# Kernel tuning notes

Measured on AMD Instinct MI355X. Metric: run time of the kernel, lower is better.

## Reference

```python
import jax, jax.numpy as jnp
import numpy as np

N_NODES = 100000
N_EDGES = 800000
F_IN, HID, N_CLS = 256, 128, 32


def setup_inputs() -> dict:
    key = jax.random.key(0)
    k1, k2, k3, k4, k5 = jax.random.split(key, 5)
    features = jax.random.normal(k1, (N_NODES, F_IN), dtype=jnp.float32)
    # random directed edges with no self loops (so add_remaining_self_loops == append all loops)
    src = jax.random.randint(k2, (N_EDGES,), 0, N_NODES)
    off = jax.random.randint(k3, (N_EDGES,), 1, N_NODES)
    dst = (src + off) % N_NODES
    edge_index = jnp.stack([src, dst]).astype(jnp.int64)
    # Glorot-style params for the two GCNConv layers
    W1 = jax.random.normal(k4, (F_IN, HID), dtype=jnp.float32) * (1.0 / np.sqrt(F_IN))
    b1 = jnp.zeros((HID,), dtype=jnp.float32)
    W2 = jax.random.normal(k5, (HID, N_CLS), dtype=jnp.float32) * (1.0 / np.sqrt(HID))
    b2 = jnp.zeros((N_CLS,), dtype=jnp.float32)
    return {"features": features, "edge_index": edge_index, "W1": W1, "b1": b1, "W2": W2, "b2": b2}


def _gcn_conv(x, W, b, src, dst, norm, n):
    xw = x @ W                                  # [N, d_out] dense GEMM
    msg = xw[src] * norm[:, None]               # gather + scale, [E, d_out]
    out = jax.ops.segment_sum(msg, dst, num_segments=n)  # scatter-add to targets
    return out + b


def reference(features, edge_index, W1, b1, W2, b2):
    n = features.shape[0]
    # add_remaining_self_loops (input has none, so append all)
    loops = jnp.arange(n, dtype=edge_index.dtype)
    src = jnp.concatenate([edge_index[0], loops])
    dst = jnp.concatenate([edge_index[1], loops])
    # gcn_norm: deg over targets, sym normalization deg^-1/2 A deg^-1/2
    deg = jax.ops.segment_sum(jnp.ones_like(src, dtype=features.dtype), dst, num_segments=n)
    dinv = jnp.where(deg > 0, jax.lax.rsqrt(deg), 0.0)
    norm = dinv[src] * dinv[dst]
    x = _gcn_conv(features, W1, b1, src, dst, norm, n)
    x = jax.nn.relu(x)
    # dropout is identity at inference (training=False)
    x = _gcn_conv(x, W2, b2, src, dst, norm, n)
    return jax.nn.log_softmax(x, axis=1)
```

## Files before the change

### kernel.cpp

```cpp
#include <hip/hip_runtime.h>
#include <hip/hip_bf16.h>

typedef __bf16 bf16_t;
typedef __attribute__((ext_vector_type(8))) __bf16 bf16x8;
typedef __attribute__((ext_vector_type(4))) float f32x4;
typedef __attribute__((ext_vector_type(2))) float f32x2;

__device__ inline void packB_one(const float* __restrict__ B, bf16_t* __restrict__ Bp,
                                 int N, int idx) {
    int j    = idx & 7;
    int lane = (idx >> 3) & 63;
    int st   = idx >> 9;
    int nt   = N >> 4;
    int s = st / nt, t = st - s * nt;
    int k = s * 32 + (lane >> 4) * 8 + j;
    int n = t * 16 + (lane & 15);
    Bp[idx] = (bf16_t)B[(size_t)k * N + n];
}

__device__ inline void fma8_fp8(uint2 u, float w, float* a) {
    f32x2 p;
    p = __builtin_amdgcn_cvt_pk_f32_fp8(u.x, false); a[0] += p[0] * w; a[1] += p[1] * w;
    p = __builtin_amdgcn_cvt_pk_f32_fp8(u.x, true);  a[2] += p[0] * w; a[3] += p[1] * w;
    p = __builtin_amdgcn_cvt_pk_f32_fp8(u.y, false); a[4] += p[0] * w; a[5] += p[1] * w;
    p = __builtin_amdgcn_cvt_pk_f32_fp8(u.y, true);  a[6] += p[0] * w; a[7] += p[1] * w;
}

__global__ __launch_bounds__(256) void k_prep(
        const float* __restrict__ W1, bf16_t* __restrict__ Bp1,
        const float* __restrict__ W2, bf16_t* __restrict__ Bp2,
        int* __restrict__ deg, int N) {
    int b = blockIdx.x, t = threadIdx.x;
    const int PACKB = (32768 + 4096) / 256;
    if (b < PACKB) {
        int idx = b * 256 + t;
        if (idx < 32768) packB_one(W1, Bp1, 128, idx);
        else             packB_one(W2, Bp2, 32, idx - 32768);
        return;
    }
    int i = ((b - PACKB) * 256 + t) * 4;
    if (i < N) {
        if (i + 4 <= N) *(int4*)(deg + i) = make_int4(0, 0, 0, 0);
        else for (int j = 0; i + j < N; ++j) deg[i + j] = 0;
    }
}

template <int KSTEPS, int NTILES>
__global__ __launch_bounds__(256) void k_front(
        const float* __restrict__ feat, const bf16_t* __restrict__ Bp1,
        unsigned char* __restrict__ XW1, int M,
        const int* __restrict__ dst, int* __restrict__ deg,
        int* __restrict__ rank, int E, int DEGB) {
    int b = blockIdx.x, t = threadIdx.x;
    if (b < DEGB) {
        int i = b * 1024 + t * 4;
        if (i + 4 <= E) {
            int4 v = *(const int4*)(dst + i);
            int4 r;
            r.x = atomicAdd(&deg[v.x], 1);
            r.y = atomicAdd(&deg[v.y], 1);
            r.z = atomicAdd(&deg[v.z], 1);
            r.w = atomicAdd(&deg[v.w], 1);
            *(int4*)(rank + i) = r;
        } else {
            for (int j = 0; j < 4; ++j)
                if (i + j < E) rank[i + j] = atomicAdd(&deg[dst[i + j]], 1);
        }
        return;
    }
    b -= DEGB;
    {
        int wave = (b * 256 + t) >> 6;
        if (wave * 16 >= M) return;
        int lane = t & 63;
        int r16 = lane & 15, quad = lane >> 4;
        const int K = KSTEPS * 32, N = NTILES * 16;
        f32x4 acc[NTILES] = {};
        const float* arow = feat + (size_t)(wave * 16 + r16) * K + quad * 8;
#pragma unroll
        for (int s = 0; s < KSTEPS; ++s) {
            const float* ap = arow + s * 32;
            bf16x8 a;
#pragma unroll
            for (int j = 0; j < 8; ++j) a[j] = (bf16_t)ap[j];
            const bf16_t* bp = Bp1 + ((size_t)(s * NTILES) * 64 + lane) * 8;
#pragma unroll
            for (int tt = 0; tt < NTILES; ++tt) {
                bf16x8 bb = *(const bf16x8*)(bp + tt * 512);
                acc[tt] = __builtin_amdgcn_mfma_f32_16x16x32_bf16(a, bb, acc[tt], 0, 0, 0);
            }
        }
#pragma unroll
        for (int tt = 0; tt < NTILES; ++tt)
#pragma unroll
            for (int r = 0; r < 4; ++r) {
                int pk = __builtin_amdgcn_cvt_pk_fp8_f32(acc[tt][r], acc[tt][r], 0, false);
                XW1[(size_t)(wave * 16 + quad * 4 + r) * N + tt * 16 + r16] =
                    (unsigned char)pk;
            }
    }
}

__global__ __launch_bounds__(256) void k_dinv_scan1(const int* __restrict__ deg,
                                                    float* __restrict__ dinv,
                                                    int* __restrict__ bsum, int n) {
    __shared__ int red[256];
    int b = blockIdx.x, t = threadIdx.x;
    int base = b * 1024 + t * 4;
    int s = 0;
#pragma unroll
    for (int j = 0; j < 4; ++j) {
        int i = base + j;
        if (i < n) { int d = deg[i]; s += d; dinv[i] = rsqrtf((float)(d + 1)); }
    }
    red[t] = s;
    __syncthreads();
    for (int d = 128; d > 0; d >>= 1) {
        if (t < d) red[t] += red[t + d];
        __syncthreads();
    }
    if (t == 0) bsum[b] = red[0];
}

__global__ __launch_bounds__(256) void k_scan3f(const int* __restrict__ deg,
                                                const int* __restrict__ bsum, int nb,
                                                int* __restrict__ rowPtr, int n) {
    __shared__ int red[256];
    __shared__ int boff[256];
    int b = blockIdx.x, t = threadIdx.x;
    int base = b * 1024 + t * 4;
    int v[4]; int s = 0;
#pragma unroll
    for (int j = 0; j < 4; ++j) { int i = base + j; v[j] = (i < n) ? deg[i] : 0; s += v[j]; }
    red[t] = s;
    boff[t] = (t < nb) ? bsum[t] : 0;
    __syncthreads();
    for (int d = 1; d < 256; d <<= 1) {
        int u  = (t >= d) ? red[t - d]  : 0;
        int u2 = (t >= d) ? boff[t - d] : 0;
        __syncthreads();
        red[t] += u;
        boff[t] += u2;
        __syncthreads();
    }
    int blockOff = (b == 0) ? 0 : boff[b - 1];
    if (b == 0 && t == 0) rowPtr[n] = boff[nb - 1];
    int run = blockOff + red[t] - s;
#pragma unroll
    for (int j = 0; j < 4; ++j) {
        int i = base + j;
        if (i < n) { rowPtr[i] = run; run += v[j]; }
    }
}

__global__ __launch_bounds__(256) void k_scatter(
        const int* __restrict__ src, const int* __restrict__ dst,
        const int* __restrict__ rank, const int* __restrict__ rowPtr,
        const float* __restrict__ dinv, int2* __restrict__ edata, int E) {
    int i = (blockIdx.x * 256 + threadIdx.x) * 4;
    if (i + 4 <= E) {
        int4 s4 = *(const int4*)(src + i);
        int4 d4 = *(const int4*)(dst + i);
        int4 r4 = *(const int4*)(rank + i);
        int p0 = rowPtr[d4.x] + r4.x, p1 = rowPtr[d4.y] + r4.y;
        int p2 = rowPtr[d4.z] + r4.z, p3 = rowPtr[d4.w] + r4.w;
        int2 e0; e0.x = s4.x; e0.y = __float_as_int(dinv[s4.x] * dinv[d4.x]);
        int2 e1; e1.x = s4.y; e1.y = __float_as_int(dinv[s4.y] * dinv[d4.y]);
        int2 e2; e2.x = s4.z; e2.y = __float_as_int(dinv[s4.z] * dinv[d4.z]);
        int2 e3; e3.x = s4.w; e3.y = __float_as_int(dinv[s4.w] * dinv[d4.w]);
        edata[p0] = e0; edata[p1] = e1; edata[p2] = e2; edata[p3] = e3;
    } else {
        for (int j = 0; j < 4; ++j) {
            int e = i + j;
            if (e >= E) break;
            int s = src[e], d = dst[e];
            int2 p; p.x = s; p.y = __float_as_int(dinv[s] * dinv[d]);
            edata[rowPtr[d] + rank[e]] = p;
        }
    }
}

template <int KSTEPS, int NTILES>
__global__ __launch_bounds__(256) void k_gemm_p(
        const bf16_t* __restrict__ Ap, const bf16_t* __restrict__ Bp,
        bf16_t* __restrict__ C, int M) {
    int wave = (blockIdx.x * blockDim.x + threadIdx.x) >> 6;
    if (wave * 16 >= M) return;
    int lane = threadIdx.x & 63;
    int r16 = lane & 15, quad = lane >> 4;
    const int N = NTILES * 16;
    f32x4 acc[NTILES] = {};
    const bf16_t* apb = Ap + (size_t)wave * (KSTEPS * 512) + lane * 8;
#pragma unroll
    for (int s = 0; s < KSTEPS; ++s) {
        bf16x8 a = *(const bf16x8*)(apb + s * 512);
        const bf16_t* bp = Bp + ((size_t)(s * NTILES) * 64 + lane) * 8;
#pragma unroll
        for (int t = 0; t < NTILES; ++t) {
            bf16x8 b = *(const bf16x8*)(bp + t * 512);
            acc[t] = __builtin_amdgcn_mfma_f32_16x16x32_bf16(a, b, acc[t], 0, 0, 0);
        }
    }
#pragma unroll
    for (int t = 0; t < NTILES; ++t)
#pragma unroll
        for (int r = 0; r < 4; ++r)
            C[(size_t)(wave * 16 + quad * 4 + r) * N + t * 16 + r16] = (bf16_t)acc[t][r];
}

__global__ __launch_bounds__(256) void k_agg1(
        const int* __restrict__ rowPtr, const int2* __restrict__ edata,
        const unsigned char* __restrict__ XW1, const float* __restrict__ dinv,
        const float* __restrict__ b1, bf16_t* __restrict__ Hp, int n) {
    int wave = (blockIdx.x * blockDim.x + threadIdx.x) >> 6;
    if (wave >= n) return;
    int lane = threadIdx.x & 63;
    int fl = (lane & 15) << 3;
    int h  = lane >> 4;
    int r0 = rowPtr[wave], r1 = rowPtr[wave + 1];
    float d = dinv[wave], d2 = d * d;
    uint2 us = *(const uint2*)(XW1 + (size_t)wave * 128 + fl);
    float a0[8] = {}, a1[8] = {};
    int k = r0 + h;
    for (; k + 4 < r1; k += 8) {
        int2 e0 = edata[k], e1 = edata[k + 4];
        float w0 = __int_as_float(e0.y), w1 = __int_as_float(e1.y);
        uint2 u0 = *(const uint2*)(XW1 + (size_t)e0.x * 128 + fl);
        uint2 u1 = *(const uint2*)(XW1 + (size_t)e1.x * 128 + fl);
        fma8_fp8(u0, w0, a0);
        fma8_fp8(u1, w1, a1);
    }
    if (k < r1) {
        int2 e0 = edata[k];
        float w0 = __int_as_float(e0.y);
        uint2 u0 = *(const uint2*)(XW1 + (size_t)e0.x * 128 + fl);
        fma8_fp8(u0, w0, a0);
    }
#pragma unroll
    for (int j = 0; j < 8; ++j) {
        a0[j] += a1[j];
        a0[j] += __shfl_xor(a0[j], 16);
        a0[j] += __shfl_xor(a0[j], 32);
    }
    if (h == 0) {
        fma8_fp8(us, d2, a0);
        bf16x8 hv;
#pragma unroll
        for (int j = 0; j < 8; ++j) {
            float v = a0[j] + b1[fl + j];
            hv[j] = (bf16_t)fmaxf(v, 0.f);
        }
        int q = lane & 15;
        size_t off = (((size_t)(wave >> 4) * 4 + (q >> 2)) * 64
                      + (wave & 15) + 16 * (q & 3)) * 8;
        *(bf16x8*)(Hp + off) = hv;
    }
}

__global__ __launch_bounds__(256) void k_agg2(
        const int* __restrict__ rowPtr, const int2* __restrict__ edata,
        const bf16_t* __restrict__ XW2, const float* __restrict__ dinv,
        const float* __restrict__ b2, float* __restrict__ out, int n) {
    int wave = (blockIdx.x * blockDim.x + threadIdx.x) >> 6;
    if (wave >= n) return;
    int lane = threadIdx.x & 63;
    int g = lane & 15;
    int h = lane >> 4;
    int r0 = rowPtr[wave], r1 = rowPtr[wave + 1];
    float d = dinv[wave], d2 = d * d;
    unsigned ps = *(const unsigned*)(XW2 + ((size_t)wave << 5) + 2 * g);
    float2 bb = *(const float2*)(b2 + 2 * g);
    float a00 = 0.f, a01 = 0.f, a10 = 0.f, a11 = 0.f;
    int k = r0 + h;
    for (; k + 4 < r1; k += 8) {
        int2 e0 = edata[k], e1 = edata[k + 4];
        float w0 = __int_as_float(e0.y), w1 = __int_as_float(e1.y);
        unsigned p0 = *(const unsigned*)(XW2 + ((size_t)e0.x << 5) + 2 * g);
        unsigned p1 = *(const unsigned*)(XW2 + ((size_t)e1.x << 5) + 2 * g);
        a00 += __int_as_float(p0 << 16) * w0;
        a01 += __int_as_float(p0 & 0xffff0000u) * w0;
        a10 += __int_as_float(p1 << 16) * w1;
        a11 += __int_as_float(p1 & 0xffff0000u) * w1;
    }
    if (k < r1) {
        int2 e0 = edata[k];
        float w0 = __int_as_float(e0.y);
        unsigned p0 = *(const unsigned*)(XW2 + ((size_t)e0.x << 5) + 2 * g);
        a00 += __int_as_float(p0 << 16) * w0;
        a01 += __int_as_float(p0 & 0xffff0000u) * w0;
    }
    float v0 = a00 + a10, v1 = a01 + a11;
    v0 += __shfl_xor(v0, 16); v0 += __shfl_xor(v0, 32);
    v1 += __shfl_xor(v1, 16); v1 += __shfl_xor(v1, 32);
    v0 += __int_as_float(ps << 16) * d2 + bb.x;
    v1 += __int_as_float(ps & 0xffff0000u) * d2 + bb.y;
    float mx = fmaxf(v0, v1);
#pragma unroll
    for (int m = 8; m >= 1; m >>= 1) mx = fmaxf(mx, __shfl_xor(mx, m));
    float s = __expf(v0 - mx) + __expf(v1 - mx);
#pragma unroll
    for (int m = 8; m >= 1; m >>= 1) s += __shfl_xor(s, m);
    if (h == 0) {
        float ls = __logf(s);
        float2 o; o.x = v0 - mx - ls; o.y = v1 - mx - ls;
        *(float2*)(out + ((size_t)wave << 5) + 2 * g) = o;
    }
}

extern "C" void kernel_launch(void* const* d_in, const int* in_sizes, int n_in,
                              void* d_out, int out_size, void* d_ws, size_t ws_size,
                              hipStream_t stream) {
    const float* feat = (const float*)d_in[0];
    const int*   eidx = (const int*)d_in[1];
    const float* W1   = (const float*)d_in[2];
    const float* b1   = (const float*)d_in[3];
    const float* W2   = (const float*)d_in[4];
    const float* b2   = (const float*)d_in[5];
    float* out = (float*)d_out;

    const int FIN = 256, HID = 128, NCLS = 32;
    const int N = in_sizes[0] / FIN;
    const int E = in_sizes[1] / 2;
    const int* src = eidx;
    const int* dst = eidx + E;

    char* ws = (char*)d_ws;
    size_t o = 0;
    auto alloc = [&](size_t bytes) -> void* {
        void* p = ws + o;
        o = (o + bytes + 255) & ~(size_t)255;
        return p;
    };
    int*    deg    = (int*)   alloc((size_t)N * 4);
    int*    rank   = (int*)   alloc((size_t)E * 4);
    float*  dinv   = (float*) alloc((size_t)N * 4);
    int*    rowPtr = (int*)   alloc((size_t)(N + 1) * 4);
    int*    bsum   = (int*)   alloc(256 * 4);
    bf16_t* Bp1    = (bf16_t*)alloc((size_t)(FIN / 32) * (HID / 16) * 512 * 2);
    bf16_t* Bp2    = (bf16_t*)alloc((size_t)(HID / 32) * (NCLS / 16) * 512 * 2);
    int2*   edata  = (int2*)  alloc((size_t)E * 8);
    unsigned char* XW1 = (unsigned char*)alloc((size_t)N * HID);
    bf16_t* Hp     = (bf16_t*)alloc((size_t)N * HID * 2);
    bf16_t* XW2    = (bf16_t*)XW1;

    const int T = 256;
    const int NB = (N + 1023) >> 10;
    const int DEGB  = (E + 1023) / 1024;
    const int GEMMB = (((N + 15) / 16) * 64 + T - 1) / T;
    const int PACKB = (32768 + 4096) / 256;
    const int ZB    = (N + 1023) / 1024;

    k_prep      <<<PACKB + ZB, T, 0, stream>>>(W1, Bp1, W2, Bp2, deg, N);
    k_front<8, 8><<<DEGB + GEMMB, T, 0, stream>>>(
        feat, Bp1, XW1, N, dst, deg, rank, E, DEGB);
    k_dinv_scan1<<<NB, T, 0, stream>>>(deg, dinv, bsum, N);
    k_scan3f    <<<NB, T, 0, stream>>>(deg, bsum, NB, rowPtr, N);
    k_scatter   <<<(E + 1023) / 1024, T, 0, stream>>>(src, dst, rank, rowPtr, dinv, edata, E);
    k_agg1<<<(N * 64 + T - 1) / T, T, 0, stream>>>(rowPtr, edata, XW1, dinv, b1, Hp, N);
    {
        int waves = (N + 15) / 16;
        k_gemm_p<4, 2><<<(waves * 64 + T - 1) / T, T, 0, stream>>>(Hp, Bp2, XW2, N);
    }
    k_agg2<<<(N * 64 + T - 1) / T, T, 0, stream>>>(rowPtr, edata, XW2, dinv, b2, out, N);
}
```

Baseline: 317.8 us.

## Privatize degree counters per XCC to use workgroup-scope atomics

Degree counting now keeps eight private copies of the degree array, one per XCC, selected by reading the hardware XCC id. The atomics run at workgroup scope so they can resolve in the local L2 instead of going device-wide. The XCC id is tagged into the high bits of each rank, and a later pass prefix-sums the per-XCC counts into offsets used during scatter. This adds an 8x larger zeroing and reading pass plus extra gathers in scatter, and it depends on workgroup-scope atomics staying coherent within one XCC's L2.

```diff
diff --git a/kernel.cpp b/kernel.cpp
--- a/kernel.cpp
+++ b/kernel.cpp
@@ -5,6 +5,15 @@
 typedef __attribute__((ext_vector_type(8))) __bf16 bf16x8;
 typedef __attribute__((ext_vector_type(4))) float f32x4;
 typedef __attribute__((ext_vector_type(2))) float f32x2;
+
+__device__ inline int xcc_id() {
+    int x;
+    asm volatile("s_getreg_b32 %0, hwreg(20, 0, 32)" : "=s"(x));
+    return x & 7;
+}
+__device__ inline int l2AtomicAdd(int* p, int v) {
+    return __hip_atomic_fetch_add(p, v, __ATOMIC_RELAXED, __HIP_MEMORY_SCOPE_WORKGROUP);
+}
 
 __device__ inline void packB_one(const float* __restrict__ B, bf16_t* __restrict__ Bp,
                                  int N, int idx) {
@@ -29,7 +38,7 @@
 __global__ __launch_bounds__(256) void k_prep(
         const float* __restrict__ W1, bf16_t* __restrict__ Bp1,
         const float* __restrict__ W2, bf16_t* __restrict__ Bp2,
-        int* __restrict__ deg, int N) {
+        int* __restrict__ deg8, int n8) {
     int b = blockIdx.x, t = threadIdx.x;
     const int PACKB = (32768 + 4096) / 256;
     if (b < PACKB) {
@@ -39,9 +48,9 @@
         return;
     }
     int i = ((b - PACKB) * 256 + t) * 4;
-    if (i < N) {
-        if (i + 4 <= N) *(int4*)(deg + i) = make_int4(0, 0, 0, 0);
-        else for (int j = 0; i + j < N; ++j) deg[i + j] = 0;
+    if (i < n8) {
+        if (i + 4 <= n8) *(int4*)(deg8 + i) = make_int4(0, 0, 0, 0);
+        else for (int j = 0; i + j < n8; ++j) deg8[i + j] = 0;
     }
 }
 
@@ -49,22 +58,25 @@
 __global__ __launch_bounds__(256) void k_front(
         const float* __restrict__ feat, const bf16_t* __restrict__ Bp1,
         unsigned char* __restrict__ XW1, int M,
-        const int* __restrict__ dst, int* __restrict__ deg,
-        int* __restrict__ rank, int E, int DEGB) {
+        const int* __restrict__ dst, int* __restrict__ deg8,
+        int* __restrict__ rank, int Nn, int E, int DEGB) {
     int b = blockIdx.x, t = threadIdx.x;
     if (b < DEGB) {
+        int x = xcc_id();
+        int* degx = deg8 + (size_t)x * Nn;
+        int tag = x << 28;
         int i = b * 1024 + t * 4;
         if (i + 4 <= E) {
             int4 v = *(const int4*)(dst + i);
             int4 r;
-            r.x = atomicAdd(&deg[v.x], 1);
-            r.y = atomicAdd(&deg[v.y], 1);
-            r.z = atomicAdd(&deg[v.z], 1);
-            r.w = atomicAdd(&deg[v.w], 1);
+            r.x = l2AtomicAdd(&degx[v.x], 1) | tag;
+            r.y = l2AtomicAdd(&degx[v.y], 1) | tag;
+            r.z = l2AtomicAdd(&degx[v.z], 1) | tag;
+            r.w = l2AtomicAdd(&degx[v.w], 1) | tag;
             *(int4*)(rank + i) = r;
         } else {
             for (int j = 0; j < 4; ++j)
-                if (i + j < E) rank[i + j] = atomicAdd(&deg[dst[i + j]], 1);
+                if (i + j < E) rank[i + j] = l2AtomicAdd(&degx[dst[i + j]], 1) | tag;
         }
         return;
     }
@@ -101,9 +113,10 @@
     }
 }
 
-__global__ __launch_bounds__(256) void k_dinv_scan1(const int* __restrict__ deg,
-                                                    float* __restrict__ dinv,
-                                                    int* __restrict__ bsum, int n) {
+__global__ __launch_bounds__(256) void k_dinv_scan1(
+        const int* __restrict__ deg8, int* __restrict__ degTot,
+        int* __restrict__ off, float* __restrict__ dinv,
+        int* __restrict__ bsum, int n) {
     __shared__ int red[256];
     int b = blockIdx.x, t = threadIdx.x;
     int base = b * 1024 + t * 4;
@@ -111,7 +124,18 @@
 #pragma unroll
     for (int j = 0; j < 4; ++j) {
         int i = base + j;
-        if (i < n) { int d = deg[i]; s += d; dinv[i] = rsqrtf((float)(d + 1)); }
+        if (i < n) {
+            int run = 0;
+#pragma unroll
+            for (int x = 0; x < 8; ++x) {
+                int v = deg8[(size_t)x * n + i];
+                off[(size_t)x * n + i] = run;
+                run += v;
+            }
+            degTot[i] = run;
+            s += run;
+            dinv[i] = rsqrtf((float)(run + 1));
+        }
     }
     red[t] = s;
     __syncthreads();
@@ -122,7 +146,7 @@
     if (t == 0) bsum[b] = red[0];
 }
 
-__global__ __launch_bounds__(256) void k_scan3f(const int* __restrict__ deg,
+__global__ __launch_bounds__(256) void k_scan3f(const int* __restrict__ degTot,
                                                 const int* __restrict__ bsum, int nb,
                                                 int* __restrict__ rowPtr, int n) {
     __shared__ int red[256];
@@ -131,7 +155,7 @@
     int base = b * 1024 + t * 4;
     int v[4]; int s = 0;
 #pragma unroll
-    for (int j = 0; j < 4; ++j) { int i = base + j; v[j] = (i < n) ? deg[i] : 0; s += v[j]; }
+    for (int j = 0; j < 4; ++j) { int i = base + j; v[j] = (i < n) ? degTot[i] : 0; s += v[j]; }
     red[t] = s;
     boff[t] = (t < nb) ? bsum[t] : 0;
     __syncthreads();
@@ -156,14 +180,17 @@
 __global__ __launch_bounds__(256) void k_scatter(
         const int* __restrict__ src, const int* __restrict__ dst,
         const int* __restrict__ rank, const int* __restrict__ rowPtr,
-        const float* __restrict__ dinv, int2* __restrict__ edata, int E) {
+        const int* __restrict__ off, const float* __restrict__ dinv,
+        int2* __restrict__ edata, int Nn, int E) {
     int i = (blockIdx.x * 256 + threadIdx.x) * 4;
     if (i + 4 <= E) {
         int4 s4 = *(const int4*)(src + i);
         int4 d4 = *(const int4*)(dst + i);
         int4 r4 = *(const int4*)(rank + i);
-        int p0 = rowPtr[d4.x] + r4.x, p1 = rowPtr[d4.y] + r4.y;
-        int p2 = rowPtr[d4.z] + r4.z, p3 = rowPtr[d4.w] + r4.w;
+        int p0 = rowPtr[d4.x] + off[(size_t)(((unsigned)r4.x) >> 28) * Nn + d4.x] + (r4.x & 0x0FFFFFFF);
+        int p1 = rowPtr[d4.y] + off[(size_t)(((unsigned)r4.y) >> 28) * Nn + d4.y] + (r4.y & 0x0FFFFFFF);
+        int p2 = rowPtr[d4.z] + off[(size_t)(((unsigned)r4.z) >> 28) * Nn + d4.z] + (r4.z & 0x0FFFFFFF);
+        int p3 = rowPtr[d4.w] + off[(size_t)(((unsigned)r4.w) >> 28) * Nn + d4.w] + (r4.w & 0x0FFFFFFF);
         int2 e0; e0.x = s4.x; e0.y = __float_as_int(dinv[s4.x] * dinv[d4.x]);
         int2 e1; e1.x = s4.y; e1.y = __float_as_int(dinv[s4.y] * dinv[d4.y]);
         int2 e2; e2.x = s4.z; e2.y = __float_as_int(dinv[s4.z] * dinv[d4.z]);
@@ -174,8 +201,9 @@
             int e = i + j;
             if (e >= E) break;
             int s = src[e], d = dst[e];
+            int r = rank[e];
             int2 p; p.x = s; p.y = __float_as_int(dinv[s] * dinv[d]);
-            edata[rowPtr[d] + rank[e]] = p;
+            edata[rowPtr[d] + off[(size_t)(((unsigned)r) >> 28) * Nn + d] + (r & 0x0FFFFFFF)] = p;
         }
     }
 }
@@ -251,9 +279,9 @@
             hv[j] = (bf16_t)fmaxf(v, 0.f);
         }
         int q = lane & 15;
-        size_t off = (((size_t)(wave >> 4) * 4 + (q >> 2)) * 64
-                      + (wave & 15) + 16 * (q & 3)) * 8;
-        *(bf16x8*)(Hp + off) = hv;
+        size_t off2 = (((size_t)(wave >> 4) * 4 + (q >> 2)) * 64
+                       + (wave & 15) + 16 * (q & 3)) * 8;
+        *(bf16x8*)(Hp + off2) = hv;
     }
 }
 
@@ -331,7 +359,9 @@
         o = (o + bytes + 255) & ~(size_t)255;
         return p;
     };
-    int*    deg    = (int*)   alloc((size_t)N * 4);
+    int*    deg8   = (int*)   alloc((size_t)8 * N * 4);
+    int*    offA   = (int*)   alloc((size_t)8 * N * 4);
+    int*    degTot = (int*)   alloc((size_t)N * 4);
     int*    rank   = (int*)   alloc((size_t)E * 4);
     float*  dinv   = (float*) alloc((size_t)N * 4);
     int*    rowPtr = (int*)   alloc((size_t)(N + 1) * 4);
@@ -348,14 +378,15 @@
     const int DEGB  = (E + 1023) / 1024;
     const int GEMMB = (((N + 15) / 16) * 64 + T - 1) / T;
     const int PACKB = (32768 + 4096) / 256;
-    const int ZB    = (N + 1023) / 1024;
-
-    k_prep      <<<PACKB + ZB, T, 0, stream>>>(W1, Bp1, W2, Bp2, deg, N);
+    const int ZB    = (8 * N / 4 + T - 1) / T;
+
+    k_prep      <<<PACKB + ZB, T, 0, stream>>>(W1, Bp1, W2, Bp2, deg8, 8 * N);
     k_front<8, 8><<<DEGB + GEMMB, T, 0, stream>>>(
-        feat, Bp1, XW1, N, dst, deg, rank, E, DEGB);
-    k_dinv_scan1<<<NB, T, 0, stream>>>(deg, dinv, bsum, N);
-    k_scan3f    <<<NB, T, 0, stream>>>(deg, bsum, NB, rowPtr, N);
-    k_scatter   <<<(E + 1023) / 1024, T, 0, stream>>>(src, dst, rank, rowPtr, dinv, edata, E);
+        feat, Bp1, XW1, N, dst, deg8, rank, N, E, DEGB);
+    k_dinv_scan1<<<NB, T, 0, stream>>>(deg8, degTot, offA, dinv, bsum, N);
+    k_scan3f    <<<NB, T, 0, stream>>>(degTot, bsum, NB, rowPtr, N);
+    k_scatter   <<<(E + 1023) / 1024, T, 0, stream>>>(
+        src, dst, rank, rowPtr, offA, dinv, edata, N, E);
     k_agg1<<<(N * 64 + T - 1) / T, T, 0, stream>>>(rowPtr, edata, XW1, dinv, b1, Hp, N);
     {
         int waves = (N + 15) / 16;
```

New measurement: 323.1 us. No clear change (+1.7%).
